# Performance work log

Hardware: AMD Instinct MI355X
Metric: run time of the kernel (lower is better)

Reference implementation:

```python
import jax, jax.numpy as jnp
import numpy as np

FEATURE_DIM = 512
Z_DIM = 256
Q_DIM = 128
NUM_Z_CODES = 4096
NUM_Q_CODES = 2048
HIDDEN_DIM = 128 * 4  # 512
BOTTLENECK = 64
BATCH = 32768


def setup_inputs() -> dict:
    key = jax.random.key(0)
    ks = jax.random.split(key, 16)
    d = {}
    d['x'] = jax.random.normal(ks[0], (BATCH, FEATURE_DIM), dtype=jnp.float32)
    # encoder: Linear(feature_dim,64) -> GELU -> Linear(64,hidden) -> GELU
    d['eW1'] = jax.random.normal(ks[1], (BOTTLENECK, FEATURE_DIM), dtype=jnp.float32) * (1.0 / np.sqrt(FEATURE_DIM))
    d['eb1'] = jnp.zeros((BOTTLENECK,), jnp.float32)
    d['eW2'] = jax.random.normal(ks[2], (HIDDEN_DIM, BOTTLENECK), dtype=jnp.float32) * (1.0 / np.sqrt(BOTTLENECK))
    d['eb2'] = jnp.zeros((HIDDEN_DIM,), jnp.float32)
    # to_z_latent LipschitzMLP(hidden, z_dim)
    d['zW'] = jax.random.normal(ks[3], (Z_DIM, HIDDEN_DIM), dtype=jnp.float32) * (1.0 / np.sqrt(HIDDEN_DIM))
    d['zb'] = jnp.zeros((Z_DIM,), jnp.float32)
    d['zci'] = jnp.ones((Z_DIM,), jnp.float32)
    # z codebook
    d['z_codebook'] = jax.random.normal(ks[4], (NUM_Z_CODES, Z_DIM), dtype=jnp.float32)
    # q_encoder LipschitzMLP(z_dim, q_dim)
    d['qW'] = jax.random.normal(ks[5], (Q_DIM, Z_DIM), dtype=jnp.float32) * (1.0 / np.sqrt(Z_DIM))
    d['qb'] = jnp.zeros((Q_DIM,), jnp.float32)
    d['qci'] = jnp.ones((Q_DIM,), jnp.float32)
    # q codebook
    d['q_codebook'] = jax.random.normal(ks[6], (NUM_Q_CODES, Q_DIM), dtype=jnp.float32)
    # decoder: Linear(q_dim,64) -> GELU -> Linear(64,hidden) -> GELU
    d['dW1'] = jax.random.normal(ks[7], (BOTTLENECK, Q_DIM), dtype=jnp.float32) * (1.0 / np.sqrt(Q_DIM))
    d['db1'] = jnp.zeros((BOTTLENECK,), jnp.float32)
    d['dW2'] = jax.random.normal(ks[8], (HIDDEN_DIM, BOTTLENECK), dtype=jnp.float32) * (1.0 / np.sqrt(BOTTLENECK))
    d['db2'] = jnp.zeros((HIDDEN_DIM,), jnp.float32)
    # to_output Linear(hidden, feature_dim)
    d['oW'] = jax.random.normal(ks[9], (FEATURE_DIM, HIDDEN_DIM), dtype=jnp.float32) * (1.0 / np.sqrt(HIDDEN_DIM))
    d['ob'] = jnp.zeros((FEATURE_DIM,), jnp.float32)
    return d


def _gelu(x):
    return jax.nn.gelu(x, approximate=False)  # torch nn.GELU default (erf)


def _lipschitz_mlp(x, W, b, ci):
    # normalization: scale each row of W so its L1 norm <= softplus(ci)
    absrowsum = jnp.sum(jnp.abs(W), axis=1, keepdims=True)          # [out,1]
    scale = jnp.minimum(1.0, jax.nn.softplus(ci)[:, None] / absrowsum)
    W_norm = W * scale
    return jax.nn.sigmoid(x @ W_norm.T + b)


def _quantize(z_e, codebook):
    # ||a-b||^2 = ||a||^2 + ||b||^2 - 2 a.b ; single big GEMM
    z_norm = jnp.sum(z_e * z_e, axis=1, keepdims=True)              # [B,1]
    cb_norm = jnp.sum(codebook * codebook, axis=1)[None, :]         # [1,K]
    dists = z_norm + cb_norm - 2.0 * (z_e @ codebook.T)             # [B,K]
    idx = jnp.argmin(dists, axis=1)
    z_q = codebook[idx]
    return z_q, idx


def _mse(a, b):
    return jnp.mean((a - b) ** 2)


def reference(x, eW1, eb1, eW2, eb2, zW, zb, zci, z_codebook,
              qW, qb, qci, q_codebook, dW1, db1, dW2, db2, oW, ob):
    sg = jax.lax.stop_gradient
    # encoder
    h = _gelu(_gelu(x @ eW1.T + eb1) @ eW2.T + eb2)                 # [B,hidden]
    z_e = _lipschitz_mlp(h, zW, zb, zci)                            # [B,z_dim]
    z_q, z_idx = _quantize(z_e, z_codebook)
    commit_z = _mse(z_e, sg(z_q))
    codebook_z = _mse(z_q, sg(z_e))
    # q level
    q_e = _lipschitz_mlp(sg(z_q), qW, qb, qci)                      # [B,q_dim]
    q_q, q_idx = _quantize(q_e, q_codebook)
    commit_q = _mse(q_e, sg(q_q))
    codebook_q = _mse(q_q, sg(q_e))
    # decoder
    dec_h = _gelu(_gelu(q_q @ dW1.T + db1) @ dW2.T + db2)           # [B,hidden]
    x_recon = dec_h @ oW.T + ob                                     # [B,feature]
    recon_loss = _mse(x_recon, x)
    loss = recon_loss + 0.25 * (commit_z + codebook_z) + 0.25 * (commit_q + codebook_q)
    return (loss, recon_loss, commit_z, codebook_z, commit_q, codebook_q,
            x_recon, z_q, q_q, z_idx, q_idx)
```

## Files before the change

### kernel.cpp

```cpp
#include <hip/hip_runtime.h>

typedef unsigned long long u64;
typedef unsigned short u16;
typedef unsigned int u32;


namespace {

constexpr int kBatch = 32768;

__device__ __forceinline__ float gelu_f(float x) {
  return 0.5f * x * (1.0f + erff(x * 0.70710678118654752440f));
}
__device__ __forceinline__ float sigmoid_f(float x) {
  return 1.0f / (1.0f + expf(-x));
}
__device__ __forceinline__ u64 pack_key(float d, unsigned j) {
  unsigned u = __float_as_uint(d);
  u = (u & 0x80000000u) ? ~u : (u | 0x80000000u);
  return ((u64)u << 32) | j;
}
__device__ __forceinline__ u16 bf16_rne(float x) {
  unsigned u = __float_as_uint(x);
  unsigned r = (u + 0x7FFFu + ((u >> 16) & 1u)) >> 16;
  return (u16)r;
}
__device__ __forceinline__ float bf16_to_f(u16 h) {
  return __uint_as_float((unsigned)h << 16);
}
__device__ __forceinline__ u64 min64(u64 a, u64 b) { return a < b ? a : b; }

__device__ __forceinline__ void load_lds16(const void* g, void* l) {
  __builtin_amdgcn_global_load_lds(
      (const __attribute__((address_space(1))) void*)g,
      (__attribute__((address_space(3))) void*)l, 16, 0, 0);
}

template <int N>
__device__ __forceinline__ void wait_vmcnt() {
  if constexpr (N == 0) {
    asm volatile("s_waitcnt vmcnt(0)" ::: "memory");
  } else if constexpr (N == 8) {
    asm volatile("s_waitcnt vmcnt(8)" ::: "memory");
  } else if constexpr (N == 16) {
    asm volatile("s_waitcnt vmcnt(16)" ::: "memory");
  }
}

__device__ __forceinline__ void lds_fence_barrier_pre() {
  asm volatile("s_waitcnt lgkmcnt(0)" ::: "memory");
  __builtin_amdgcn_sched_barrier(0);
  __builtin_amdgcn_s_barrier();
  asm volatile("" ::: "memory");
  __builtin_amdgcn_sched_barrier(0);
}

__device__ __forceinline__ void barrier_raw() {
  __builtin_amdgcn_sched_barrier(0);
  __builtin_amdgcn_s_barrier();
  asm volatile("" ::: "memory");
  __builtin_amdgcn_sched_barrier(0);
}

typedef short bf16x8 __attribute__((ext_vector_type(8)));
typedef float f32x4 __attribute__((ext_vector_type(4)));

__global__ void prep_cb_kernel(const float* __restrict__ zcb,
                               u16* __restrict__ zcbh, float* __restrict__ zcbn,
                               const float* __restrict__ qcb,
                               u16* __restrict__ qcbh, float* __restrict__ qcbn) {
  int b = blockIdx.x;
  const float* cb;
  u16* cbh;
  float* cbn;
  int K;
  if (b < 1024) { cb = zcb; cbh = zcbh; cbn = zcbn; K = 256; }
  else { b -= 1024; cb = qcb; cbh = qcbh; cbn = qcbn; K = 128; }
  const int row = b * 4 + (threadIdx.x >> 6);
  const int lane = threadIdx.x & 63;
  double s = 0.0;
  for (int k = lane; k < K; k += 64) {
    const float v = cb[(size_t)row * K + k];
    cbh[(size_t)row * K + k] = bf16_rne(v);
    s += (double)v * (double)v;
  }
#pragma unroll
  for (int o = 32; o > 0; o >>= 1) s += __shfl_down(s, o);
  if (lane == 0) cbn[row] = (float)s;
}

__global__ void prep_w_kernel(
    const float* __restrict__ zW, const float* __restrict__ zci,
    const float* __restrict__ qW, const float* __restrict__ qci,
    const float* __restrict__ eW1, const float* __restrict__ eW2,
    u16* __restrict__ zWns, u16* __restrict__ qWns, u16* __restrict__ eW1s,
    u16* __restrict__ eW2s, const float* __restrict__ dW1,
    const float* __restrict__ dW2, const float* __restrict__ oW,
    u16* __restrict__ dW1b, u16* __restrict__ dW2b, u16* __restrict__ oWb) {
  const int b = blockIdx.x;
  const int tid = threadIdx.x;
  if (b < 384) {
    const float* W;
    const float* ci;
    u16* D;
    int K, row;
    if (b < 256) { W = zW; ci = zci; D = zWns; K = 512; row = b; }
    else { W = qW; ci = qci; D = qWns; K = 256; row = b - 256; }
    float s = 0.f;
    for (int k = tid; k < K; k += 256) s += fabsf(W[(size_t)row * K + k]);
#pragma unroll
    for (int o = 32; o > 0; o >>= 1) s += __shfl_down(s, o);
    __shared__ float p[4];
    if ((tid & 63) == 0) p[tid >> 6] = s;
    __syncthreads();
    const float tot = p[0] + p[1] + p[2] + p[3];
    const float c = ci[row];
    const float sp = (c > 20.f) ? c : log1pf(expf(c));
    const float scale = fminf(1.f, sp / tot);
    for (int k = tid; k < K; k += 256) {
      const float v = W[(size_t)row * K + k] * scale;
      const u16 h = bf16_rne(v);
      const u16 l = bf16_rne(v - bf16_to_f(h));
      D[(size_t)row * 3 * K + k] = h;
      D[(size_t)row * 3 * K + K + k] = h;
      D[(size_t)row * 3 * K + 2 * K + k] = l;
    }
  } else if (b < 512) {
    const int i = (b - 384) * 256 + tid;
    const int r = i >> 9, k = i & 511;
    const float v = eW1[i];
    const u16 h = bf16_rne(v);
    const u16 l = bf16_rne(v - bf16_to_f(h));
    eW1s[(size_t)r * 1536 + k] = h;
    eW1s[(size_t)r * 1536 + 512 + k] = h;
    eW1s[(size_t)r * 1536 + 1024 + k] = l;
  } else if (b < 640) {
    const int i = (b - 512) * 256 + tid;
    const int r = i >> 6, k = i & 63;
    const float v = eW2[i];
    const u16 h = bf16_rne(v);
    const u16 l = bf16_rne(v - bf16_to_f(h));
    eW2s[(size_t)r * 192 + k] = h;
    eW2s[(size_t)r * 192 + 64 + k] = h;
    eW2s[(size_t)r * 192 + 128 + k] = l;
  } else if (b < 672) {
    const int i = (b - 640) * 256 + tid;
    dW1b[i] = bf16_rne(dW1[i]);
  } else if (b < 800) {
    const int i = (b - 672) * 256 + tid;
    dW2b[i] = bf16_rne(dW2[i]);
  } else {
    const int i = (b - 800) * 256 + tid;
    oWb[i] = bf16_rne(oW[i]);
  }
}

__global__ void cast_split_x_kernel(const float* __restrict__ x,
                                    u16* __restrict__ xs) {
  const int i = blockIdx.x * 256 + threadIdx.x;
  const int row = i >> 7, c4 = i & 127;
  const float4 v = *(const float4*)(x + (size_t)row * 512 + c4 * 4);
  const float vv[4] = {v.x, v.y, v.z, v.w};
  u16 hv[4], lv[4];
#pragma unroll
  for (int j = 0; j < 4; ++j) {
    hv[j] = bf16_rne(vv[j]);
    lv[j] = bf16_rne(vv[j] - bf16_to_f(hv[j]));
  }
  *(ushort4*)(xs + (size_t)row * 1024 + c4 * 4) =
      make_ushort4(hv[0], hv[1], hv[2], hv[3]);
  *(ushort4*)(xs + (size_t)row * 1024 + 512 + c4 * 4) =
      make_ushort4(lv[0], lv[1], lv[2], lv[3]);
}

enum { U_GELU_SPLIT = 0, U_SIG_SPLIT = 1, U_GELU_B16 = 2, U_RECON = 3 };

template <int TM, int TN, int NW, int MODE>
__global__ __launch_bounds__(NW * 64) void gemm_uni(
    const u16* __restrict__ A, const u16* __restrict__ B,
    const float* __restrict__ bias, void* __restrict__ Cv,
    const float* __restrict__ X, float* __restrict__ psum, int Ktot,
    int wrapA, int strideA, int N) {
  __shared__ __align__(16) u16 As[TM * 64];
  __shared__ __align__(16) u16 Bs[TN * 64];
  constexpr int NT = NW * 64;
  constexpr int AIT = (TM * 8) / NT;
  constexpr int BIT = (TN * 8) / NT;
  const int tid = threadIdx.x;
  const int lane = tid & 63, w = tid >> 6;
  const int quad = lane >> 4, l15 = lane & 15;
  const int waveM = (TN == 64) ? w * 64 : (w & 1) * 64;
  const int waveN = (TN == 64) ? 0 : (w >> 1) * 64;
  const int rowBase = blockIdx.y * TM;
  const int colBase = blockIdx.x * TN;

  f32x4 acc[4][4] = {};

  for (int k0 = 0; k0 < Ktot; k0 += 64) {
    const int sk0 = (k0 >= wrapA) ? k0 - wrapA : k0;
    __syncthreads();
#pragma unroll
    for (int i = 0; i < AIT; ++i) {
      const int ch = i * NT + tid;
      const int r = ch >> 3, c = ch & 7, g = c ^ (r & 7);
      load_lds16(A + (size_t)(rowBase + r) * strideA + sk0 + g * 8,
                 (char*)As + ch * 16);
    }
#pragma unroll
    for (int i = 0; i < BIT; ++i) {
      const int ch = i * NT + tid;
      const int r = ch >> 3, c = ch & 7, g = c ^ (r & 7);
      load_lds16(B + (size_t)(colBase + r) * Ktot + k0 + g * 8,
                 (char*)Bs + ch * 16);
    }
    __syncthreads();
#pragma unroll
    for (int ks = 0; ks < 2; ++ks) {
      bf16x8 af[4], bf[4];
      const int ch = ks * 4 + quad;
#pragma unroll
      for (int mi = 0; mi < 4; ++mi) {
        const int rl = waveM + mi * 16 + l15;
        af[mi] = *(const bf16x8*)(As + rl * 64 + (ch ^ (rl & 7)) * 8);
      }
#pragma unroll
      for (int ni = 0; ni < 4; ++ni) {
        const int rl = waveN + ni * 16 + l15;
        bf[ni] = *(const bf16x8*)(Bs + rl * 64 + (ch ^ (rl & 7)) * 8);
      }
#pragma unroll
      for (int mi = 0; mi < 4; ++mi)
#pragma unroll
        for (int ni = 0; ni < 4; ++ni)
          acc[mi][ni] = __builtin_amdgcn_mfma_f32_16x16x32_bf16(
              af[mi], bf[ni], acc[mi][ni], 0, 0, 0);
    }
  }

  if constexpr (MODE == U_GELU_SPLIT || MODE == U_SIG_SPLIT) {
    u16* S = (u16*)Cv;
#pragma unroll
    for (int mi = 0; mi < 4; ++mi)
#pragma unroll
      for (int r = 0; r < 4; ++r) {
        const int row = rowBase + waveM + mi * 16 + quad * 4 + r;
#pragma unroll
        for (int ni = 0; ni < 4; ++ni) {
          const int col = colBase + waveN + ni * 16 + l15;
          const float pre = acc[mi][ni][r] + bias[col];
          const float v = (MODE == U_GELU_SPLIT) ? gelu_f(pre) : sigmoid_f(pre);
          const u16 h = bf16_rne(v);
          const u16 l = bf16_rne(v - bf16_to_f(h));
          S[(size_t)row * 2 * N + col] = h;
          S[(size_t)row * 2 * N + N + col] = l;
        }
      }
  } else if constexpr (MODE == U_GELU_B16) {
    u16* C = (u16*)Cv;
#pragma unroll
    for (int mi = 0; mi < 4; ++mi)
#pragma unroll
      for (int r = 0; r < 4; ++r) {
        const int row = rowBase + waveM + mi * 16 + quad * 4 + r;
#pragma unroll
        for (int ni = 0; ni < 4; ++ni) {
          const int col = colBase + waveN + ni * 16 + l15;
          C[(size_t)row * N + col] =
              bf16_rne(gelu_f(acc[mi][ni][r] + bias[col]));
        }
      }
  } else {
    float* C = (float*)Cv;
    float local = 0.f;
#pragma unroll
    for (int mi = 0; mi < 4; ++mi)
#pragma unroll
      for (int r = 0; r < 4; ++r) {
        const int row = rowBase + waveM + mi * 16 + quad * 4 + r;
#pragma unroll
        for (int ni = 0; ni < 4; ++ni) {
          const int col = colBase + waveN + ni * 16 + l15;
          const float val = acc[mi][ni][r] + bias[col];
          const float d = val - X[(size_t)row * N + col];
          local += d * d;
          C[(size_t)row * N + col] = val;
        }
      }
#pragma unroll
    for (int o = 32; o > 0; o >>= 1) local += __shfl_down(local, o);
    __shared__ float psh[NW];
    if (lane == 0) psh[w] = local;
    __syncthreads();
    if (tid == 0) {
      float t = 0.f;
#pragma unroll
      for (int i = 0; i < NW; ++i) t += psh[i];
      psum[blockIdx.y * gridDim.x + blockIdx.x] = t;
    }
  }
}

template <int KT, int BTG>
__global__ __launch_bounds__(512, 2) void dist2p8_kernel(
    const u16* __restrict__ CB, const u16* __restrict__ ZB,
    const float* __restrict__ cbn, u32* __restrict__ cand, int strideB,
    int nx) {
  constexpr int CH = KT / 8;
  constexpr int KSTEPS = KT / 32;
  constexpr int SLOTS = (128 * CH) / 512;
  __shared__ __align__(16) u16 bufC[128 * KT];
  __shared__ __align__(16) u16 bufB[128 * KT];
  __shared__ u32 wred[128 * 4];
  const int tid = threadIdx.x;
  const int lane = tid & 63, w = tid >> 6;
  const int quad = lane >> 4, l15 = lane & 15;
  const int waveM = (w & 1) * 64;
  const int waveN = (w >> 1) * 32;
  const int ct = blockIdx.y;
  const int btg = blockIdx.x;
  const int codeBase = ct * 128;

  float cnf[4][4];
#pragma unroll
  for (int mi = 0; mi < 4; ++mi)
#pragma unroll
    for (int r = 0; r < 4; ++r)
      cnf[mi][r] =
          cbn[codeBase + waveM + mi * 16 + quad * 4 + r] * 512.0f + 131072.0f;
  asm volatile("" ::: "memory");

#pragma unroll
  for (int i = 0; i < SLOTS; ++i) {
    const int ch = i * 512 + tid;
    const int r = ch / CH, c = ch % CH, g = c ^ (r & 7);
    load_lds16(CB + (size_t)(codeBase + r) * KT + g * 8, (char*)bufC + ch * 16);
  }
  wait_vmcnt<0>();
  barrier_raw();

  for (int bt = 0; bt < BTG; ++bt) {
    const int rowBase = (btg * BTG + bt) * 128;
#pragma unroll
    for (int i = 0; i < SLOTS; ++i) {
      const int ch = i * 512 + tid;
      const int r = ch / CH, c = ch % CH, g = c ^ (r & 7);
      load_lds16(ZB + (size_t)(rowBase + r) * strideB + g * 8,
                 (char*)bufB + ch * 16);
    }
    wait_vmcnt<0>();
    barrier_raw();

    f32x4 acc[4][2] = {};
#pragma unroll
    for (int kk = 0; kk < KSTEPS; ++kk) {
      bf16x8 af[4], bf[2];
#pragma unroll
      for (int mi = 0; mi < 4; ++mi) {
        const int rl = waveM + mi * 16 + l15;
        const int sw = (kk * 4 + quad) ^ (rl & 7);
        af[mi] = *(const bf16x8*)(bufC + rl * KT + sw * 8);
      }
#pragma unroll
      for (int ni = 0; ni < 2; ++ni) {
        const int rn = waveN + ni * 16 + l15;
        const int sw = (kk * 4 + quad) ^ (rn & 7);
        bf[ni] = *(const bf16x8*)(bufB + rn * KT + sw * 8);
      }
#pragma unroll
      for (int mi = 0; mi < 4; ++mi)
#pragma unroll
        for (int ni = 0; ni < 2; ++ni)
          acc[mi][ni] = __builtin_amdgcn_mfma_f32_16x16x32_bf16(
              af[mi], bf[ni], acc[mi][ni], 0, 0, 0);
    }

#pragma unroll
    for (int ni = 0; ni < 2; ++ni) {
      u32 b0 = ~0u, b1 = ~0u;
#pragma unroll
      for (int mi = 0; mi < 4; ++mi)
#pragma unroll
        for (int r = 0; r < 4; ++r) {
          const float kf = fmaf(acc[mi][ni][r], -1024.0f, cnf[mi][r]);
          u32 iv = (u32)kf;
          iv = iv > 0xFFFFFu ? 0xFFFFFu : iv;
          const u32 key =
              (iv << 12) | (codeBase + waveM + mi * 16 + quad * 4 + r);
          if (key < b0) { b1 = b0; b0 = key; }
          else if (key < b1) { b1 = key; }
        }
#pragma unroll
      for (int off = 16; off < 64; off <<= 1) {
        const u32 o0 = __shfl_xor(b0, off);
        const u32 o1 = __shfl_xor(b1, off);
        const u32 n0 = min(b0, o0);
        const u32 n1 = min(max(b0, o0), min(b1, o1));
        b0 = n0; b1 = n1;
      }
      if (quad == 0) {
        const int rloc = waveN + ni * 16 + l15;
        wred[rloc * 4 + (w & 1) * 2 + 0] = b0;
        wred[rloc * 4 + (w & 1) * 2 + 1] = b1;
      }
    }
    lds_fence_barrier_pre();
    if (tid < 128) {
      const u32 a0 = wred[tid * 4 + 0], a1 = wred[tid * 4 + 1];
      const u32 c0 = wred[tid * 4 + 2], c1 = wred[tid * 4 + 3];
      const u32 b0 = min(a0, c0);
      const u32 b1 = min(max(a0, c0), min(a1, c1));
      u32* dst = cand + (size_t)(rowBase + tid) * (2 * nx) + 2 * ct;
      *(u64*)dst = ((u64)b1 << 32) | b0;
    }
  }
}

template <int KT, int BTG>
__global__ __launch_bounds__(256) void dist2p_kernel(
    const u16* __restrict__ CB, const u16* __restrict__ ZB,
    const float* __restrict__ cbn, u32* __restrict__ cand, int strideB,
    int nx) {
  constexpr int CH = KT / 8;
  constexpr int KSTEPS = KT / 32;
  constexpr int SLOTS = (128 * CH) / 256;
  __shared__ __align__(16) u16 bufA[128 * KT];
  __shared__ __align__(16) u16 bufB[128 * KT];
  __shared__ u32 wred[128 * 4];
  const int tid = threadIdx.x;
  const int lane = tid & 63, w = tid >> 6;
  const int quad = lane >> 4, l15 = lane & 15;
  const int waveM = (w & 1) * 64;
  const int waveN = (w >> 1) * 64;
  const int ct = blockIdx.y;
  const int btg = blockIdx.x;
  const int codeBase = ct * 128;

  float cnf[4][4];
#pragma unroll
  for (int mi = 0; mi < 4; ++mi)
#pragma unroll
    for (int r = 0; r < 4; ++r)
      cnf[mi][r] =
          cbn[codeBase + waveM + mi * 16 + quad * 4 + r] * 512.0f + 131072.0f;
  asm volatile("" ::: "memory");

#pragma unroll
  for (int i = 0; i < SLOTS; ++i) {
    const int ch = i * 256 + tid;
    const int r = ch / CH, c = ch % CH, g = c ^ (r & 7);
    load_lds16(CB + (size_t)(codeBase + r) * KT + g * 8, (char*)bufA + ch * 16);
  }
  {
    const int rowBase0 = btg * BTG * 128;
#pragma unroll
    for (int i = 0; i < SLOTS; ++i) {
      const int ch = i * 256 + tid;
      const int r = ch / CH, c = ch % CH, g = c ^ (r & 7);
      load_lds16(ZB + (size_t)(rowBase0 + r) * strideB + g * 8,
                 (char*)bufB + ch * 16);
    }
  }
  wait_vmcnt<SLOTS>();
  barrier_raw();

  bf16x8 af[KSTEPS][4];
#pragma unroll
  for (int kk = 0; kk < KSTEPS; ++kk)
#pragma unroll
    for (int mi = 0; mi < 4; ++mi) {
      const int rl = waveM + mi * 16 + l15;
      const int sw = (kk * 4 + quad) ^ (rl & 7);
      af[kk][mi] = *(const bf16x8*)(bufA + rl * KT + sw * 8);
    }
  lds_fence_barrier_pre();

  for (int bt = 0; bt < BTG; ++bt) {
    const int rowBase = (btg * BTG + bt) * 128;
    const u16* curp = (bt & 1) ? bufA : bufB;
    u16* nxtp = (bt & 1) ? bufB : bufA;

    if (bt + 1 < BTG) {
#pragma unroll
      for (int i = 0; i < SLOTS; ++i) {
        const int ch = i * 256 + tid;
        const int r = ch / CH, c = ch % CH, g = c ^ (r & 7);
        load_lds16(ZB + (size_t)(rowBase + 128 + r) * strideB + g * 8,
                   (char*)nxtp + ch * 16);
      }
      wait_vmcnt<SLOTS>();
    } else {
      wait_vmcnt<0>();
    }
    barrier_raw();

    f32x4 acc[4][4] = {};
#pragma unroll
    for (int kk = 0; kk < KSTEPS; ++kk) {
      bf16x8 bf[4];
#pragma unroll
      for (int ni = 0; ni < 4; ++ni) {
        const int rn = waveN + ni * 16 + l15;
        const int sw = (kk * 4 + quad) ^ (rn & 7);
        bf[ni] = *(const bf16x8*)(curp + rn * KT + sw * 8);
      }
#pragma unroll
      for (int mi = 0; mi < 4; ++mi)
#pragma unroll
        for (int ni = 0; ni < 4; ++ni)
          acc[mi][ni] = __builtin_amdgcn_mfma_f32_16x16x32_bf16(
              af[kk][mi], bf[ni], acc[mi][ni], 0, 0, 0);
    }

#pragma unroll
    for (int ni = 0; ni < 4; ++ni) {
      u32 b0 = ~0u, b1 = ~0u;
#pragma unroll
      for (int mi = 0; mi < 4; ++mi)
#pragma unroll
        for (int r = 0; r < 4; ++r) {
          const float kf = fmaf(acc[mi][ni][r], -1024.0f, cnf[mi][r]);
          u32 iv = (u32)kf;
          iv = iv > 0xFFFFFu ? 0xFFFFFu : iv;
          const u32 key =
              (iv << 12) | (codeBase + waveM + mi * 16 + quad * 4 + r);
          if (key < b0) { b1 = b0; b0 = key; }
          else if (key < b1) { b1 = key; }
        }
#pragma unroll
      for (int off = 16; off < 64; off <<= 1) {
        const u32 o0 = __shfl_xor(b0, off);
        const u32 o1 = __shfl_xor(b1, off);
        const u32 n0 = min(b0, o0);
        const u32 n1 = min(max(b0, o0), min(b1, o1));
        b0 = n0; b1 = n1;
      }
      if (quad == 0) {
        const int rloc = waveN + ni * 16 + l15;
        wred[rloc * 4 + (w & 1) * 2 + 0] = b0;
        wred[rloc * 4 + (w & 1) * 2 + 1] = b1;
      }
    }
    lds_fence_barrier_pre();
    if (tid < 128) {
      const u32 a0 = wred[tid * 4 + 0], a1 = wred[tid * 4 + 1];
      const u32 c0 = wred[tid * 4 + 2], c1 = wred[tid * 4 + 3];
      const u32 b0 = min(a0, c0);
      const u32 b1 = min(max(a0, c0), min(a1, c1));
      u32* dst = cand + (size_t)(rowBase + tid) * (2 * nx) + 2 * ct;
      *(u64*)dst = ((u64)b1 << 32) | b0;
    }
  }
}

template <int K, int NC, int LEVEL>
__global__ __launch_bounds__(256, 4) void rerank_kernel(
    const u32* __restrict__ cand, const u16* __restrict__ zes,
    const float* __restrict__ cb, const float* __restrict__ cbn,
    float* __restrict__ outq, u16* __restrict__ wsq,
    float* __restrict__ out_idx, float* __restrict__ psum) {
  constexpr int DV = K / 32;
  constexpr int MV = K / 64;
  const int w = threadIdx.x >> 6, lane = threadIdx.x & 63;
  const int row = blockIdx.x * 4 + w;
  const int g = lane >> 3, sub = lane & 7;

  const u16* zr = zes + (size_t)row * 2 * K;

  ushort4 zh[DV], zl[DV];
#pragma unroll
  for (int i = 0; i < DV; ++i) {
    zh[i] = *(const ushort4*)(zr + sub * (K / 8) + 4 * i);
    zl[i] = *(const ushort4*)(zr + K + sub * (K / 8) + 4 * i);
  }
  float zmse[MV];
#pragma unroll
  for (int i = 0; i < MV; ++i) {
    const int c = lane + 64 * i;
    zmse[i] = bf16_to_f(zr[c]) + bf16_to_f(zr[K + c]);
  }
  const u32 mykey = (lane < NC) ? cand[(size_t)row * NC + lane] : ~0u;

  __shared__ u32 kb[4][72];
  kb[w][lane] = mykey;
  __syncthreads();
  int rank = 0;
#pragma unroll
  for (int j = 0; j < 64; ++j) {
    const u32 kj = kb[w][j];
    rank += (kj < mykey || (kj == mykey && j < lane)) ? 1 : 0;
  }
  if (rank < 8) kb[w][64 + rank] = mykey;
  __syncthreads();
  const unsigned ci = kb[w][64 + g] & 0xFFFu;

  const float* cr = cb + (size_t)ci * K;
  float dot = 0.f;
#pragma unroll
  for (int i = 0; i < DV; ++i) {
    const float4 cv = *(const float4*)(cr + sub * (K / 8) + 4 * i);
    dot = fmaf(bf16_to_f(zh[i].x) + bf16_to_f(zl[i].x), cv.x, dot);
    dot = fmaf(bf16_to_f(zh[i].y) + bf16_to_f(zl[i].y), cv.y, dot);
    dot = fmaf(bf16_to_f(zh[i].z) + bf16_to_f(zl[i].z), cv.z, dot);
    dot = fmaf(bf16_to_f(zh[i].w) + bf16_to_f(zl[i].w), cv.w, dot);
  }
#pragma unroll
  for (int off = 1; off < 8; off <<= 1) dot += __shfl_xor(dot, off);
  u64 k2 = pack_key(cbn[ci] - 2.0f * dot, ci);
#pragma unroll
  for (int off = 8; off < 64; off <<= 1) k2 = min64(k2, __shfl_xor(k2, off));
  const unsigned best = (unsigned)k2;
  if (lane == 0) out_idx[row] = (float)best;

  const float* br = cb + (size_t)best * K;
  float local = 0.f;
#pragma unroll
  for (int i = 0; i < MV; ++i) {
    const int c = lane + 64 * i;
    const float v = br[c];
    const float d = zmse[i] - v;
    local += d * d;
    outq[(size_t)row * K + c] = v;
    if (LEVEL == 0) {
      const u16 h = bf16_rne(v);
      wsq[(size_t)row * 2 * K + c] = h;
      wsq[(size_t)row * 2 * K + K + c] = bf16_rne(v - bf16_to_f(h));
    } else {
      wsq[(size_t)row * K + c] = bf16_rne(v);
    }
  }
#pragma unroll
  for (int o = 32; o > 0; o >>= 1) local += __shfl_down(local, o);
  __shared__ float p[4];
  if (lane == 0) p[w] = local;
  __syncthreads();
  if (threadIdx.x == 0) psum[blockIdx.x] = p[0] + p[1] + p[2] + p[3];
}

__global__ void finalize_kernel(const float* __restrict__ psumZ,
                                const float* __restrict__ psumQ,
                                const float* __restrict__ psumR,
                                float* __restrict__ out) {
  const int tid = threadIdx.x;
  float sz = 0.f, sq = 0.f, sr = 0.f;
  for (int i = tid; i < 8192; i += 256) {
    sz += psumZ[i];
    sq += psumQ[i];
  }
  for (int i = tid; i < 1024; i += 256) sr += psumR[i];
#pragma unroll
  for (int o = 32; o > 0; o >>= 1) {
    sz += __shfl_down(sz, o);
    sq += __shfl_down(sq, o);
    sr += __shfl_down(sr, o);
  }
  __shared__ float pz[4], pq[4], pr[4];
  if ((tid & 63) == 0) {
    pz[tid >> 6] = sz;
    pq[tid >> 6] = sq;
    pr[tid >> 6] = sr;
  }
  __syncthreads();
  if (tid == 0) {
    const float cz = (pz[0] + pz[1] + pz[2] + pz[3]) / ((float)kBatch * 256.f);
    const float cq = (pq[0] + pq[1] + pq[2] + pq[3]) / ((float)kBatch * 128.f);
    const float rec = (pr[0] + pr[1] + pr[2] + pr[3]) / ((float)kBatch * 512.f);
    out[0] = rec + 0.5f * cz + 0.5f * cq;
    out[1] = rec;
    out[2] = cz;
    out[3] = cz;
    out[4] = cq;
    out[5] = cq;
  }
}

}

extern "C" void kernel_launch(void* const* d_in, const int* in_sizes, int n_in,
                              void* d_out, int out_size, void* d_ws,
                              size_t ws_size, hipStream_t stream) {
  const float* x   = (const float*)d_in[0];
  const float* eW1 = (const float*)d_in[1];
  const float* eb1 = (const float*)d_in[2];
  const float* eW2 = (const float*)d_in[3];
  const float* eb2 = (const float*)d_in[4];
  const float* zW  = (const float*)d_in[5];
  const float* zb  = (const float*)d_in[6];
  const float* zci = (const float*)d_in[7];
  const float* zcb = (const float*)d_in[8];
  const float* qW  = (const float*)d_in[9];
  const float* qb  = (const float*)d_in[10];
  const float* qci = (const float*)d_in[11];
  const float* qcb = (const float*)d_in[12];
  const float* dW1 = (const float*)d_in[13];
  const float* db1 = (const float*)d_in[14];
  const float* dW2 = (const float*)d_in[15];
  const float* db2 = (const float*)d_in[16];
  const float* oW  = (const float*)d_in[17];
  const float* ob  = (const float*)d_in[18];

  float* out = (float*)d_out;
  float* out_xr = out + 6;
  float* out_zq = out_xr + (size_t)32768 * 512;
  float* out_qq = out_zq + (size_t)32768 * 256;
  float* out_zi = out_qq + (size_t)32768 * 128;
  float* out_qi = out_zi + 32768;

  char* wsb = (char*)d_ws;
  u16*  zWns = (u16*) (wsb + 0x0000000);
  u16*  qWns = (u16*) (wsb + 0x00C0000);
  u16*  eW1s = (u16*) (wsb + 0x00F0000);
  u16*  eW2s = (u16*) (wsb + 0x0120000);
  u16*  dW1b = (u16*) (wsb + 0x0150000);
  u16*  dW2b = (u16*) (wsb + 0x0154000);
  u16*  oWb  = (u16*) (wsb + 0x0164000);
  u16*  zcbh = (u16*) (wsb + 0x01E4000);
  u16*  qcbh = (u16*) (wsb + 0x03E4000);
  float* zcbn = (float*)(wsb + 0x0464000);
  float* qcbn = (float*)(wsb + 0x0468000);
  float* psumR = (float*)(wsb + 0x046B000);
  float* psumZ = (float*)(wsb + 0x0470000);
  float* psumQ = (float*)(wsb + 0x0478000);
  u16*  h1s  = (u16*) (wsb + 0x0480000);
  u16*  h1b  = (u16*) (wsb + 0x0480000);
  u16*  zes  = (u16*) (wsb + 0x0C80000);
  u16*  qes  = (u16*) (wsb + 0x0C80000);
  u16*  hb   = (u16*) (wsb + 0x0C80000);
  u16*  xs   = (u16*) (wsb + 0x2C80000);
  u16*  hs   = (u16*) (wsb + 0x2C80000);
  u32*  candz = (u32*)(wsb + 0x2C80000);
  u16*  zqs  = (u16*) (wsb + 0x3480000);
  u32*  candq = (u32*)(wsb + 0x2C80000);
  u16*  qqb  = (u16*) (wsb + 0x5480000);

  prep_cb_kernel<<<1536, 256, 0, stream>>>(zcb, zcbh, zcbn, qcb, qcbh, qcbn);
  prep_w_kernel<<<1824, 256, 0, stream>>>(zW, zci, qW, qci, eW1, eW2, zWns,
                                          qWns, eW1s, eW2s, dW1, dW2, oW,
                                          dW1b, dW2b, oWb);
  cast_split_x_kernel<<<16384, 256, 0, stream>>>(x, xs);

  gemm_uni<128, 64, 2, U_GELU_SPLIT><<<dim3(1, 256), 128, 0, stream>>>(
      xs, eW1s, eb1, h1s, nullptr, nullptr, 1536, 1024, 1024, 64);
  gemm_uni<128, 128, 4, U_GELU_SPLIT><<<dim3(4, 256), 256, 0, stream>>>(
      h1s, eW2s, eb2, hs, nullptr, nullptr, 192, 128, 128, 512);
  gemm_uni<128, 128, 4, U_SIG_SPLIT><<<dim3(2, 256), 256, 0, stream>>>(
      hs, zWns, zb, zes, nullptr, nullptr, 1536, 1024, 1024, 256);

  dist2p8_kernel<256, 32><<<dim3(8, 32), 512, 0, stream>>>(
      zcbh, zes, zcbn, candz, 512, 32);
  rerank_kernel<256, 64, 0><<<8192, 256, 0, stream>>>(
      candz, zes, zcb, zcbn, out_zq, zqs, out_zi, psumZ);

  gemm_uni<128, 128, 4, U_SIG_SPLIT><<<dim3(1, 256), 256, 0, stream>>>(
      zqs, qWns, qb, qes, nullptr, nullptr, 768, 512, 512, 128);
  dist2p_kernel<128, 8><<<dim3(32, 16), 256, 0, stream>>>(
      qcbh, qes, qcbn, candq, 256, 16);
  rerank_kernel<128, 32, 1><<<8192, 256, 0, stream>>>(
      candq, qes, qcb, qcbn, out_qq, qqb, out_qi, psumQ);

  gemm_uni<128, 64, 2, U_GELU_B16><<<dim3(1, 256), 128, 0, stream>>>(
      qqb, dW1b, db1, h1b, nullptr, nullptr, 128, 1 << 30, 128, 64);
  gemm_uni<128, 128, 4, U_GELU_B16><<<dim3(4, 256), 256, 0, stream>>>(
      h1b, dW2b, db2, hb, nullptr, nullptr, 64, 1 << 30, 64, 512);
  gemm_uni<128, 128, 4, U_RECON><<<dim3(4, 256), 256, 0, stream>>>(
      hb, oWb, ob, out_xr, x, psumR, 512, 1 << 30, 512, 512);

  finalize_kernel<<<1, 256, 0, stream>>>(psumZ, psumQ, psumR, out);

  (void)in_sizes; (void)n_in; (void)out_size; (void)ws_size;
}
```

Baseline: 696.8 us.

## Software-pipeline z-codebook distance kernel: overlap top-2 epilogue with next tile MFMAs

Replaces the 512-thread z-level distance kernel with a 256-thread variant in which each wave computes a 64x64 tile, doubling its per-wave work. Accumulators are double-buffered so the top-2 key selection for the previous batch tile is interleaved into the MFMA loop of the current tile. The next Z tile is staged into LDS while the shuffle reduction runs. The aim is to hide epilogue ALU and load latency behind matrix work, at the cost of many more accumulator registers and lower occupancy.

```diff
diff --git a/kernel.cpp b/kernel.cpp
--- a/kernel.cpp
+++ b/kernel.cpp
@@ -301,13 +301,13 @@
 }
 
 template <int KT, int BTG>
-__global__ __launch_bounds__(512, 2) void dist2p8_kernel(
+__global__ __launch_bounds__(256) void dist2pp_kernel(
     const u16* __restrict__ CB, const u16* __restrict__ ZB,
     const float* __restrict__ cbn, u32* __restrict__ cand, int strideB,
     int nx) {
   constexpr int CH = KT / 8;
   constexpr int KSTEPS = KT / 32;
-  constexpr int SLOTS = (128 * CH) / 512;
+  constexpr int SLOTS = (128 * CH) / 256;
   __shared__ __align__(16) u16 bufC[128 * KT];
   __shared__ __align__(16) u16 bufB[128 * KT];
   __shared__ u32 wred[128 * 4];
@@ -315,7 +315,7 @@
   const int lane = tid & 63, w = tid >> 6;
   const int quad = lane >> 4, l15 = lane & 15;
   const int waveM = (w & 1) * 64;
-  const int waveN = (w >> 1) * 32;
+  const int waveN = (w >> 1) * 64;
   const int ct = blockIdx.y;
   const int btg = blockIdx.x;
   const int codeBase = ct * 128;
@@ -331,29 +331,33 @@
 
 #pragma unroll
   for (int i = 0; i < SLOTS; ++i) {
-    const int ch = i * 512 + tid;
+    const int ch = i * 256 + tid;
     const int r = ch / CH, c = ch % CH, g = c ^ (r & 7);
     load_lds16(CB + (size_t)(codeBase + r) * KT + g * 8, (char*)bufC + ch * 16);
   }
+  {
+    const int rowBase0 = btg * BTG * 128;
+#pragma unroll
+    for (int i = 0; i < SLOTS; ++i) {
+      const int ch = i * 256 + tid;
+      const int r = ch / CH, c = ch % CH, g = c ^ (r & 7);
+      load_lds16(ZB + (size_t)(rowBase0 + r) * strideB + g * 8,
+                 (char*)bufB + ch * 16);
+    }
+  }
   wait_vmcnt<0>();
   barrier_raw();
 
-  for (int bt = 0; bt < BTG; ++bt) {
-    const int rowBase = (btg * BTG + bt) * 128;
-#pragma unroll
-    for (int i = 0; i < SLOTS; ++i) {
-      const int ch = i * 512 + tid;
-      const int r = ch / CH, c = ch % CH, g = c ^ (r & 7);
-      load_lds16(ZB + (size_t)(rowBase + r) * strideB + g * 8,
-                 (char*)bufB + ch * 16);
-    }
-    wait_vmcnt<0>();
-    barrier_raw();
-
-    f32x4 acc[4][2] = {};
+  f32x4 accA[4][4], accB[4][4];
+
+  {
+#pragma unroll
+    for (int mi = 0; mi < 4; ++mi)
+#pragma unroll
+      for (int ni = 0; ni < 4; ++ni) accA[mi][ni] = f32x4{0.f, 0.f, 0.f, 0.f};
 #pragma unroll
     for (int kk = 0; kk < KSTEPS; ++kk) {
-      bf16x8 af[4], bf[2];
+      bf16x8 af[4], bf[4];
 #pragma unroll
       for (int mi = 0; mi < 4; ++mi) {
         const int rl = waveM + mi * 16 + l15;
@@ -361,7 +365,7 @@
         af[mi] = *(const bf16x8*)(bufC + rl * KT + sw * 8);
       }
 #pragma unroll
-      for (int ni = 0; ni < 2; ++ni) {
+      for (int ni = 0; ni < 4; ++ni) {
         const int rn = waveN + ni * 16 + l15;
         const int sw = (kk * 4 + quad) ^ (rn & 7);
         bf[ni] = *(const bf16x8*)(bufB + rn * KT + sw * 8);
@@ -369,26 +373,83 @@
 #pragma unroll
       for (int mi = 0; mi < 4; ++mi)
 #pragma unroll
-        for (int ni = 0; ni < 2; ++ni)
-          acc[mi][ni] = __builtin_amdgcn_mfma_f32_16x16x32_bf16(
-              af[mi], bf[ni], acc[mi][ni], 0, 0, 0);
-    }
-
-#pragma unroll
-    for (int ni = 0; ni < 2; ++ni) {
-      u32 b0 = ~0u, b1 = ~0u;
+        for (int ni = 0; ni < 4; ++ni)
+          accA[mi][ni] = __builtin_amdgcn_mfma_f32_16x16x32_bf16(
+              af[mi], bf[ni], accA[mi][ni], 0, 0, 0);
+    }
+    lds_fence_barrier_pre();
+    const int rowBase1 = (btg * BTG + 1) * 128;
+#pragma unroll
+    for (int i = 0; i < SLOTS; ++i) {
+      const int ch = i * 256 + tid;
+      const int r = ch / CH, c = ch % CH, g = c ^ (r & 7);
+      load_lds16(ZB + (size_t)(rowBase1 + r) * strideB + g * 8,
+                 (char*)bufB + ch * 16);
+    }
+    wait_vmcnt<0>();
+    barrier_raw();
+  }
+
+  auto body = [&](f32x4(&cur)[4][4], f32x4(&prev)[4][4], int t, bool doStage) {
+    u32 pb0[4], pb1[4];
+#pragma unroll
+    for (int ni = 0; ni < 4; ++ni) { pb0[ni] = ~0u; pb1[ni] = ~0u; }
+#pragma unroll
+    for (int mi = 0; mi < 4; ++mi)
+#pragma unroll
+      for (int ni = 0; ni < 4; ++ni) cur[mi][ni] = f32x4{0.f, 0.f, 0.f, 0.f};
+#pragma unroll
+    for (int kk = 0; kk < KSTEPS; ++kk) {
+      bf16x8 af[4], bf[4];
+#pragma unroll
+      for (int mi = 0; mi < 4; ++mi) {
+        const int rl = waveM + mi * 16 + l15;
+        const int sw = (kk * 4 + quad) ^ (rl & 7);
+        af[mi] = *(const bf16x8*)(bufC + rl * KT + sw * 8);
+      }
+#pragma unroll
+      for (int ni = 0; ni < 4; ++ni) {
+        const int rn = waveN + ni * 16 + l15;
+        const int sw = (kk * 4 + quad) ^ (rn & 7);
+        bf[ni] = *(const bf16x8*)(bufB + rn * KT + sw * 8);
+      }
 #pragma unroll
       for (int mi = 0; mi < 4; ++mi)
 #pragma unroll
+        for (int ni = 0; ni < 4; ++ni)
+          cur[mi][ni] = __builtin_amdgcn_mfma_f32_16x16x32_bf16(
+              af[mi], bf[ni], cur[mi][ni], 0, 0, 0);
+      const int nie = kk >> 1;
+#pragma unroll
+      for (int m2 = 0; m2 < 2; ++m2) {
+        const int mi = (kk & 1) * 2 + m2;
+#pragma unroll
         for (int r = 0; r < 4; ++r) {
-          const float kf = fmaf(acc[mi][ni][r], -1024.0f, cnf[mi][r]);
+          const float kf = fmaf(prev[mi][nie][r], -1024.0f, cnf[mi][r]);
           u32 iv = (u32)kf;
           iv = iv > 0xFFFFFu ? 0xFFFFFu : iv;
           const u32 key =
               (iv << 12) | (codeBase + waveM + mi * 16 + quad * 4 + r);
-          if (key < b0) { b1 = b0; b0 = key; }
-          else if (key < b1) { b1 = key; }
+          if (key < pb0[nie]) { pb1[nie] = pb0[nie]; pb0[nie] = key; }
+          else if (key < pb1[nie]) { pb1[nie] = key; }
         }
+      }
+    }
+    lds_fence_barrier_pre();
+
+    if (doStage) {
+      const int rowBaseN = (btg * BTG + t + 1) * 128;
+#pragma unroll
+      for (int i = 0; i < SLOTS; ++i) {
+        const int ch = i * 256 + tid;
+        const int r = ch / CH, c = ch % CH, g = c ^ (r & 7);
+        load_lds16(ZB + (size_t)(rowBaseN + r) * strideB + g * 8,
+                   (char*)bufB + ch * 16);
+      }
+    }
+#pragma unroll
+    for (int ni = 0; ni < 4; ++ni) {
+      u32 b0 = pb0[ni], b1 = pb1[ni];
 #pragma unroll
       for (int off = 16; off < 64; off <<= 1) {
         const u32 o0 = __shfl_xor(b0, off);
@@ -403,13 +464,70 @@
         wred[rloc * 4 + (w & 1) * 2 + 1] = b1;
       }
     }
+    wait_vmcnt<0>();
     lds_fence_barrier_pre();
     if (tid < 128) {
+      const int rowBaseS = (btg * BTG + t - 1) * 128;
       const u32 a0 = wred[tid * 4 + 0], a1 = wred[tid * 4 + 1];
       const u32 c0 = wred[tid * 4 + 2], c1 = wred[tid * 4 + 3];
       const u32 b0 = min(a0, c0);
       const u32 b1 = min(max(a0, c0), min(a1, c1));
-      u32* dst = cand + (size_t)(rowBase + tid) * (2 * nx) + 2 * ct;
+      u32* dst = cand + (size_t)(rowBaseS + tid) * (2 * nx) + 2 * ct;
+      *(u64*)dst = ((u64)b1 << 32) | b0;
+    }
+  };
+
+#pragma unroll 1
+  for (int p = 0; p < BTG / 2 - 1; ++p) {
+    body(accB, accA, 2 * p + 1, true);
+    body(accA, accB, 2 * p + 2, true);
+  }
+  body(accB, accA, BTG - 1, false);
+
+  {
+    u32 fb0[4], fb1[4];
+#pragma unroll
+    for (int ni = 0; ni < 4; ++ni) { fb0[ni] = ~0u; fb1[ni] = ~0u; }
+#pragma unroll
+    for (int ni = 0; ni < 4; ++ni)
+#pragma unroll
+      for (int mi = 0; mi < 4; ++mi)
+#pragma unroll
+        for (int r = 0; r < 4; ++r) {
+          const float kf = fmaf(accB[mi][ni][r], -1024.0f, cnf[mi][r]);
+          u32 iv = (u32)kf;
+          iv = iv > 0xFFFFFu ? 0xFFFFFu : iv;
+          const u32 key =
+              (iv << 12) | (codeBase + waveM + mi * 16 + quad * 4 + r);
+          if (key < fb0[ni]) { fb1[ni] = fb0[ni]; fb0[ni] = key; }
+          else if (key < fb1[ni]) { fb1[ni] = key; }
+        }
+    lds_fence_barrier_pre();
+#pragma unroll
+    for (int ni = 0; ni < 4; ++ni) {
+      u32 b0 = fb0[ni], b1 = fb1[ni];
+#pragma unroll
+      for (int off = 16; off < 64; off <<= 1) {
+        const u32 o0 = __shfl_xor(b0, off);
+        const u32 o1 = __shfl_xor(b1, off);
+        const u32 n0 = min(b0, o0);
+        const u32 n1 = min(max(b0, o0), min(b1, o1));
+        b0 = n0; b1 = n1;
+      }
+      if (quad == 0) {
+        const int rloc = waveN + ni * 16 + l15;
+        wred[rloc * 4 + (w & 1) * 2 + 0] = b0;
+        wred[rloc * 4 + (w & 1) * 2 + 1] = b1;
+      }
+    }
+    lds_fence_barrier_pre();
+    if (tid < 128) {
+      const int rowBaseS = (btg * BTG + BTG - 1) * 128;
+      const u32 a0 = wred[tid * 4 + 0], a1 = wred[tid * 4 + 1];
+      const u32 c0 = wred[tid * 4 + 2], c1 = wred[tid * 4 + 3];
+      const u32 b0 = min(a0, c0);
+      const u32 b1 = min(max(a0, c0), min(a1, c1));
+      u32* dst = cand + (size_t)(rowBaseS + tid) * (2 * nx) + 2 * ct;
       *(u64*)dst = ((u64)b1 << 32) | b0;
     }
   }
@@ -745,7 +863,7 @@
   gemm_uni<128, 128, 4, U_SIG_SPLIT><<<dim3(2, 256), 256, 0, stream>>>(
       hs, zWns, zb, zes, nullptr, nullptr, 1536, 1024, 1024, 256);
 
-  dist2p8_kernel<256, 32><<<dim3(8, 32), 512, 0, stream>>>(
+  dist2pp_kernel<256, 32><<<dim3(8, 32), 256, 0, stream>>>(
       zcbh, zes, zcbn, candz, 512, 32);
   rerank_kernel<256, 64, 0><<<8192, 256, 0, stream>>>(
       candz, zes, zcb, zcbn, out_zq, zqs, out_zi, psumZ);
```

Result: slower. 975.2 us (+40.0%).

## Retile z-distance kernel with register-resident codebook fragments and prefetched batch tiles

Applied to the files above, without the earlier changes.

Replaces the 512-thread z-codebook distance kernel with a 256-thread kernel using 64-code by 64-row tiles. The codebook fragments are loaded once into registers, and the next batch tile's LDS load is issued right after the reduction barrier, overlapping it with the candidate write. Each code tile now keeps only its top-1 candidate instead of top-2; there are twice as many tiles, so the reranker still receives 64 candidates per row. The trade-off is higher register pressure and a different candidate set, which may affect rerank accuracy.

```diff
diff --git a/kernel.cpp b/kernel.cpp
--- a/kernel.cpp
+++ b/kernel.cpp
@@ -300,29 +300,30 @@
   }
 }
 
-template <int KT, int BTG>
-__global__ __launch_bounds__(512, 2) void dist2p8_kernel(
+template <int KT, int CT, int BR, int BTG>
+__global__ __launch_bounds__(256) void dist2z_kernel(
     const u16* __restrict__ CB, const u16* __restrict__ ZB,
     const float* __restrict__ cbn, u32* __restrict__ cand, int strideB,
-    int nx) {
+    int ncand) {
   constexpr int CH = KT / 8;
   constexpr int KSTEPS = KT / 32;
-  constexpr int SLOTS = (128 * CH) / 512;
-  __shared__ __align__(16) u16 bufC[128 * KT];
-  __shared__ __align__(16) u16 bufB[128 * KT];
-  __shared__ u32 wred[128 * 4];
+  constexpr int CSLOTS = (CT * CH) / 256;
+  constexpr int BSLOTS = (BR * CH) / 256;
+  __shared__ __align__(16) u16 bufC[CT * KT];
+  __shared__ __align__(16) u16 bufB[BR * KT];
+  __shared__ u32 wred[BR * 2];
   const int tid = threadIdx.x;
   const int lane = tid & 63, w = tid >> 6;
   const int quad = lane >> 4, l15 = lane & 15;
-  const int waveM = (w & 1) * 64;
+  const int waveM = (w & 1) * 32;
   const int waveN = (w >> 1) * 32;
   const int ct = blockIdx.y;
   const int btg = blockIdx.x;
-  const int codeBase = ct * 128;
-
-  float cnf[4][4];
-#pragma unroll
-  for (int mi = 0; mi < 4; ++mi)
+  const int codeBase = ct * CT;
+
+  float cnf[2][4];
+#pragma unroll
+  for (int mi = 0; mi < 2; ++mi)
 #pragma unroll
     for (int r = 0; r < 4; ++r)
       cnf[mi][r] =
@@ -330,36 +331,42 @@
   asm volatile("" ::: "memory");
 
 #pragma unroll
-  for (int i = 0; i < SLOTS; ++i) {
-    const int ch = i * 512 + tid;
+  for (int i = 0; i < CSLOTS; ++i) {
+    const int ch = i * 256 + tid;
     const int r = ch / CH, c = ch % CH, g = c ^ (r & 7);
     load_lds16(CB + (size_t)(codeBase + r) * KT + g * 8, (char*)bufC + ch * 16);
   }
+  {
+    const int rowBase0 = btg * BTG * BR;
+#pragma unroll
+    for (int i = 0; i < BSLOTS; ++i) {
+      const int ch = i * 256 + tid;
+      const int r = ch / CH, c = ch % CH, g = c ^ (r & 7);
+      load_lds16(ZB + (size_t)(rowBase0 + r) * strideB + g * 8,
+                 (char*)bufB + ch * 16);
+    }
+  }
   wait_vmcnt<0>();
   barrier_raw();
 
+  bf16x8 af[KSTEPS][2];
+#pragma unroll
+  for (int kk = 0; kk < KSTEPS; ++kk)
+#pragma unroll
+    for (int mi = 0; mi < 2; ++mi) {
+      const int rl = waveM + mi * 16 + l15;
+      const int sw = (kk * 4 + quad) ^ (rl & 7);
+      af[kk][mi] = *(const bf16x8*)(bufC + rl * KT + sw * 8);
+    }
+
+#pragma unroll 1
   for (int bt = 0; bt < BTG; ++bt) {
-    const int rowBase = (btg * BTG + bt) * 128;
-#pragma unroll
-    for (int i = 0; i < SLOTS; ++i) {
-      const int ch = i * 512 + tid;
-      const int r = ch / CH, c = ch % CH, g = c ^ (r & 7);
-      load_lds16(ZB + (size_t)(rowBase + r) * strideB + g * 8,
-                 (char*)bufB + ch * 16);
-    }
-    wait_vmcnt<0>();
-    barrier_raw();
-
-    f32x4 acc[4][2] = {};
+    const int rowBase = (btg * BTG + bt) * BR;
+
+    f32x4 acc[2][2] = {};
 #pragma unroll
     for (int kk = 0; kk < KSTEPS; ++kk) {
-      bf16x8 af[4], bf[2];
-#pragma unroll
-      for (int mi = 0; mi < 4; ++mi) {
-        const int rl = waveM + mi * 16 + l15;
-        const int sw = (kk * 4 + quad) ^ (rl & 7);
-        af[mi] = *(const bf16x8*)(bufC + rl * KT + sw * 8);
-      }
+      bf16x8 bf[2];
 #pragma unroll
       for (int ni = 0; ni < 2; ++ni) {
         const int rn = waveN + ni * 16 + l15;
@@ -367,18 +374,18 @@
         bf[ni] = *(const bf16x8*)(bufB + rn * KT + sw * 8);
       }
 #pragma unroll
-      for (int mi = 0; mi < 4; ++mi)
+      for (int mi = 0; mi < 2; ++mi)
 #pragma unroll
         for (int ni = 0; ni < 2; ++ni)
           acc[mi][ni] = __builtin_amdgcn_mfma_f32_16x16x32_bf16(
-              af[mi], bf[ni], acc[mi][ni], 0, 0, 0);
+              af[kk][mi], bf[ni], acc[mi][ni], 0, 0, 0);
     }
 
 #pragma unroll
     for (int ni = 0; ni < 2; ++ni) {
-      u32 b0 = ~0u, b1 = ~0u;
-#pragma unroll
-      for (int mi = 0; mi < 4; ++mi)
+      u32 b0 = ~0u;
+#pragma unroll
+      for (int mi = 0; mi < 2; ++mi)
 #pragma unroll
         for (int r = 0; r < 4; ++r) {
           const float kf = fmaf(acc[mi][ni][r], -1024.0f, cnf[mi][r]);
@@ -386,32 +393,33 @@
           iv = iv > 0xFFFFFu ? 0xFFFFFu : iv;
           const u32 key =
               (iv << 12) | (codeBase + waveM + mi * 16 + quad * 4 + r);
-          if (key < b0) { b1 = b0; b0 = key; }
-          else if (key < b1) { b1 = key; }
+          b0 = min(b0, key);
         }
-#pragma unroll
-      for (int off = 16; off < 64; off <<= 1) {
-        const u32 o0 = __shfl_xor(b0, off);
-        const u32 o1 = __shfl_xor(b1, off);
-        const u32 n0 = min(b0, o0);
-        const u32 n1 = min(max(b0, o0), min(b1, o1));
-        b0 = n0; b1 = n1;
-      }
+      b0 = min(b0, (u32)__shfl_xor(b0, 16));
+      b0 = min(b0, (u32)__shfl_xor(b0, 32));
       if (quad == 0) {
         const int rloc = waveN + ni * 16 + l15;
-        wred[rloc * 4 + (w & 1) * 2 + 0] = b0;
-        wred[rloc * 4 + (w & 1) * 2 + 1] = b1;
+        wred[rloc * 2 + (w & 1)] = b0;
       }
     }
     lds_fence_barrier_pre();
-    if (tid < 128) {
-      const u32 a0 = wred[tid * 4 + 0], a1 = wred[tid * 4 + 1];
-      const u32 c0 = wred[tid * 4 + 2], c1 = wred[tid * 4 + 3];
-      const u32 b0 = min(a0, c0);
-      const u32 b1 = min(max(a0, c0), min(a1, c1));
-      u32* dst = cand + (size_t)(rowBase + tid) * (2 * nx) + 2 * ct;
-      *(u64*)dst = ((u64)b1 << 32) | b0;
-    }
+
+    if (bt + 1 < BTG) {
+      const int rowBaseN = rowBase + BR;
+#pragma unroll
+      for (int i = 0; i < BSLOTS; ++i) {
+        const int ch = i * 256 + tid;
+        const int r = ch / CH, c = ch % CH, g = c ^ (r & 7);
+        load_lds16(ZB + (size_t)(rowBaseN + r) * strideB + g * 8,
+                   (char*)bufB + ch * 16);
+      }
+    }
+    if (tid < BR) {
+      const u32 m0 = min(wred[tid * 2 + 0], wred[tid * 2 + 1]);
+      cand[(size_t)(rowBase + tid) * ncand + ct] = m0;
+    }
+    wait_vmcnt<0>();
+    lds_fence_barrier_pre();
   }
 }
 
@@ -745,8 +753,8 @@
   gemm_uni<128, 128, 4, U_SIG_SPLIT><<<dim3(2, 256), 256, 0, stream>>>(
       hs, zWns, zb, zes, nullptr, nullptr, 1536, 1024, 1024, 256);
 
-  dist2p8_kernel<256, 32><<<dim3(8, 32), 512, 0, stream>>>(
-      zcbh, zes, zcbn, candz, 512, 32);
+  dist2z_kernel<256, 64, 64, 64><<<dim3(8, 64), 256, 0, stream>>>(
+      zcbh, zes, zcbn, candz, 512, 64);
   rerank_kernel<256, 64, 0><<<8192, 256, 0, stream>>>(
       candz, zes, zcb, zcbn, out_zq, zqs, out_zi, psumZ);
 
```

Result: no change. 689.5 us (-1.0%).
